# Optimization experiments

Measured on AMD Instinct MI355X. Metric: run time of the kernel, lower is better.

The kernel has to match this reference:

```python
import jax, jax.numpy as jnp
import numpy as np

B, C, H, W, A = 64, 1280, 7, 7, 40  # batch, in_features, spatial, num_attr


def h_swish(x):
    # x * relu6(x + 3) / 6
    return x * jnp.clip(x + 3.0, 0.0, 6.0) * (1.0 / 6.0)


def setup_inputs() -> dict:
    key = jax.random.key(0)
    kx, k1, k2, k3, k4 = jax.random.split(key, 5)
    s1 = 1.0 / np.sqrt(C)
    return {
        "x": jax.random.normal(kx, (B, C, H, W), dtype=jnp.float32),
        # batched per-attribute head params: Linear(C,C) then Linear(C,1)
        "W1": jax.random.uniform(k1, (A, C, C), jnp.float32, -s1, s1),
        "b1": jax.random.uniform(k2, (A, C), jnp.float32, -s1, s1),
        "W2": jax.random.uniform(k3, (A, C), jnp.float32, -s1, s1),
        "b2": jax.random.uniform(k4, (A,), jnp.float32, -s1, s1),
    }


def reference(x, W1, b1, W2, b2):
    # AdaptiveAvgPool2d((1,1)) + h_swish, then flatten -> [B, C]
    p = h_swish(jnp.mean(x, axis=(2, 3)))
    # all per-attribute heads as one batched GEMM: [B,C] x [A,C,C] -> [B,A,C]
    h = h_swish(jnp.einsum("bc,acd->bad", p, W1) + b1)
    # second layer: Linear(C,1) per attr -> [B, A]
    out = jnp.einsum("bac,ac->ba", h, W2) + b2
    # eval mode (self.training == False): sigmoid applied, dropout inactive
    return jax.nn.sigmoid(out)
```

## Files before the change

kernel.cpp:

```cpp
#include <hip/hip_runtime.h>
#include <hip/hip_bf16.h>

#define B_    64
#define C_    1280
#define HW_   49
#define A_    40
#define BN    128
#define BK    64
#define NKT   (C_/BK)
#define NTILE (C_/BN)

typedef short bf16x8 __attribute__((ext_vector_type(8)));
typedef float f32x4  __attribute__((ext_vector_type(4)));

__device__ __forceinline__ float hswish(float x) {
    float t = fminf(fmaxf(x + 3.0f, 0.0f), 6.0f);
    return x * t * (1.0f / 6.0f);
}

__device__ __forceinline__ short f2bf(float f) {
    __hip_bfloat16 h = __float2bfloat16(f);
    return __builtin_bit_cast(short, h);
}

__device__ __forceinline__ int swz(int r, int k) {
    return r * BK + ((((k >> 3) ^ r) & 7) << 3) + (k & 7);
}

#define POOL_ROWS 64
__global__ __launch_bounds__(256) void pool_kernel(const float* __restrict__ x,
                                                   __hip_bfloat16* __restrict__ p) {
    __shared__ float buf[POOL_ROWS * HW_];
    const int tid = threadIdx.x;
    const size_t base = (size_t)blockIdx.x * (POOL_ROWS * HW_);
    const float4* src = reinterpret_cast<const float4*>(x + base);
    #pragma unroll
    for (int i = 0; i < 3; ++i) {
        float4 v = src[tid + i * 256];
        *reinterpret_cast<float4*>(&buf[(tid + i * 256) * 4]) = v;
    }
    if (tid < 16) {
        float4 v = src[768 + tid];
        *reinterpret_cast<float4*>(&buf[(768 + tid) * 4]) = v;
    }
    __syncthreads();
    if (tid < POOL_ROWS) {
        float s = 0.f;
        #pragma unroll
        for (int j = 0; j < HW_; ++j) s += buf[tid * HW_ + j];
        s *= (1.0f / 49.0f);
        p[blockIdx.x * POOL_ROWS + tid] = __float2bfloat16(hswish(s));
    }
}

__global__ __launch_bounds__(256) void head_kernel(
    const short* __restrict__ p,
    const float* __restrict__ W1,
    const float* __restrict__ b1,
    const float* __restrict__ W2,
    float* __restrict__ part)
{
    __shared__ short w_lds[BN * BK];
    __shared__ short p_lds[B_ * BK];

    const int tid  = threadIdx.x;
    const int lane = tid & 63;
    const int wid  = tid >> 6;
    const int ntile = blockIdx.x;
    const int a     = blockIdx.y;
    const int n0    = ntile * BN;

    const int l15 = lane & 15;
    const int lg  = lane >> 4;

    const int sd = tid & 127;
    const int kh = (tid >> 7) * 32;
    const float* w1base = W1 + (size_t)a * C_ * C_ + n0 + sd;

    const int pr = tid & 63;
    const int ks = (tid >> 6) * 16;
    const short* pbase = p + (size_t)pr * C_ + ks;

    f32x4 acc[8];
    #pragma unroll
    for (int n = 0; n < 8; ++n) acc[n] = (f32x4){0.f, 0.f, 0.f, 0.f};

    float  wraw[32];
    bf16x8 praw[2];

#define LOADW(KT) do {                                              \
        const float* _wb = w1base + (size_t)((KT) * BK + kh) * C_;  \
        _Pragma("unroll")                                           \
        for (int _i = 0; _i < 32; ++_i)                             \
            wraw[_i] = _wb[(size_t)_i * C_];                        \
    } while (0)

#define LOADP(KT) do {                                              \
        const short* _pb = pbase + (KT) * BK;                       \
        praw[0] = *reinterpret_cast<const bf16x8*>(_pb);            \
        praw[1] = *reinterpret_cast<const bf16x8*>(_pb + 8);        \
    } while (0)

    LOADW(0); LOADP(0);

    for (int kt = 0; kt < NKT; ++kt) {
        __syncthreads();
        #pragma unroll
        for (int i = 0; i < 4; ++i) {
            bf16x8 v;
            #pragma unroll
            for (int j = 0; j < 8; ++j) v[j] = f2bf(wraw[i * 8 + j]);
            *reinterpret_cast<bf16x8*>(&w_lds[swz(sd, kh + i * 8)]) = v;
        }
        *reinterpret_cast<bf16x8*>(&p_lds[swz(pr, ks)])     = praw[0];
        *reinterpret_cast<bf16x8*>(&p_lds[swz(pr, ks + 8)]) = praw[1];
        __syncthreads();

        if (kt + 1 < NKT) { LOADW(kt + 1); LOADP(kt + 1); }

        #pragma unroll
        for (int h = 0; h < 2; ++h) {
            bf16x8 afrag = *reinterpret_cast<const bf16x8*>(
                &p_lds[swz(wid * 16 + l15, h * 32 + lg * 8)]);
            #pragma unroll
            for (int n = 0; n < 8; ++n) {
                bf16x8 bfrag = *reinterpret_cast<const bf16x8*>(
                    &w_lds[swz(n * 16 + l15, h * 32 + lg * 8)]);
                acc[n] = __builtin_amdgcn_mfma_f32_16x16x32_bf16(afrag, bfrag, acc[n], 0, 0, 0);
            }
        }
    }
#undef LOADW
#undef LOADP

    float partial[4] = {0.f, 0.f, 0.f, 0.f};
    #pragma unroll
    for (int n = 0; n < 8; ++n) {
        int col = n0 + n * 16 + l15;
        float b1v = b1[a * C_ + col];
        float w2v = W2[a * C_ + col];
        #pragma unroll
        for (int r = 0; r < 4; ++r)
            partial[r] += hswish(acc[n][r] + b1v) * w2v;
    }
    #pragma unroll
    for (int off = 8; off >= 1; off >>= 1)
        #pragma unroll
        for (int r = 0; r < 4; ++r)
            partial[r] += __shfl_xor(partial[r], off, 64);
    if (l15 == 0) {
        int brow = wid * 16 + lg * 4;
        #pragma unroll
        for (int r = 0; r < 4; ++r)
            part[ntile * (B_ * A_) + (brow + r) * A_ + a] = partial[r];
    }
}

__global__ __launch_bounds__(256) void fin_kernel(const float* __restrict__ part,
                                                  const float* __restrict__ b2,
                                                  float* __restrict__ out) {
    int idx = blockIdx.x * 256 + threadIdx.x;
    if (idx >= B_ * A_) return;
    int a = idx % A_;
    float s = b2[a];
    #pragma unroll
    for (int nb = 0; nb < NTILE; ++nb) s += part[nb * (B_ * A_) + idx];
    out[idx] = 1.0f / (1.0f + expf(-s));
}

extern "C" void kernel_launch(void* const* d_in, const int* in_sizes, int n_in,
                              void* d_out, int out_size, void* d_ws, size_t ws_size,
                              hipStream_t stream) {
    const float* x  = (const float*)d_in[0];
    const float* W1 = (const float*)d_in[1];
    const float* b1 = (const float*)d_in[2];
    const float* W2 = (const float*)d_in[3];
    const float* b2 = (const float*)d_in[4];
    float* out = (float*)d_out;

    __hip_bfloat16* p = (__hip_bfloat16*)d_ws;
    float* part = (float*)((char*)d_ws + (size_t)B_ * C_ * 2);

    pool_kernel<<<(B_ * C_) / POOL_ROWS, 256, 0, stream>>>(x, p);
    head_kernel<<<dim3(NTILE, A_), 256, 0, stream>>>((const short*)p, W1, b1, W2, part);
    fin_kernel<<<(B_ * A_ + 255) / 256, 256, 0, stream>>>(part, b2, out);
}
```

Measured before the change: 59.12 us.

## Halve head tile width and double-buffer register prefetch of W1 tiles

Narrows the N tile of the head GEMM from 128 to 64 columns, which doubles the grid to 800 blocks, and splits the register staging into two alternating buffers so global loads for two K-tiles ahead are in flight while the current tile is computed. Syncthreads is replaced by raw s_barrier plus an explicit lgkmcnt wait, and the per-wave partial sums are staged through a small LDS buffer before being written out. The goal is more memory-level parallelism on this bandwidth-bound fp32 weight stream. The cost is higher register pressure from the dropped launch bound, twice as many partial tiles for the final reduction, and barrier correctness that now depends on the manual waits.

```diff
diff --git a/kernel.cpp b/kernel.cpp
--- a/kernel.cpp
+++ b/kernel.cpp
@@ -5,7 +5,7 @@
 #define C_    1280
 #define HW_   49
 #define A_    40
-#define BN    128
+#define BN    64
 #define BK    64
 #define NKT   (C_/BK)
 #define NTILE (C_/BN)
@@ -53,7 +53,7 @@
     }
 }
 
-__global__ __launch_bounds__(256) void head_kernel(
+__global__ void head_kernel(
     const short* __restrict__ p,
     const float* __restrict__ W1,
     const float* __restrict__ b1,
@@ -62,6 +62,7 @@
 {
     __shared__ short w_lds[BN * BK];
     __shared__ short p_lds[B_ * BK];
+    __shared__ float red[4][B_];
 
     const int tid  = threadIdx.x;
     const int lane = tid & 63;
@@ -73,69 +74,86 @@
     const int l15 = lane & 15;
     const int lg  = lane >> 4;
 
-    const int sd = tid & 127;
-    const int kh = (tid >> 7) * 32;
+    const int sd = tid & 63;
+    const int kq = (tid >> 6) * 16;
     const float* w1base = W1 + (size_t)a * C_ * C_ + n0 + sd;
 
     const int pr = tid & 63;
     const int ks = (tid >> 6) * 16;
     const short* pbase = p + (size_t)pr * C_ + ks;
 
-    f32x4 acc[8];
-    #pragma unroll
-    for (int n = 0; n < 8; ++n) acc[n] = (f32x4){0.f, 0.f, 0.f, 0.f};
-
-    float  wraw[32];
-    bf16x8 praw[2];
-
-#define LOADW(KT) do {                                              \
-        const float* _wb = w1base + (size_t)((KT) * BK + kh) * C_;  \
+    f32x4 acc[4];
+    #pragma unroll
+    for (int n = 0; n < 4; ++n) acc[n] = (f32x4){0.f, 0.f, 0.f, 0.f};
+
+    float  wrawA[16], wrawB[16];
+    bf16x8 prawA[2], prawB[2];
+
+#define LOADW(KT, BUF) do {                                         \
+        const float* _wb = w1base + (size_t)((KT) * BK + kq) * C_;  \
         _Pragma("unroll")                                           \
-        for (int _i = 0; _i < 32; ++_i)                             \
-            wraw[_i] = _wb[(size_t)_i * C_];                        \
-    } while (0)
-
-#define LOADP(KT) do {                                              \
+        for (int _i = 0; _i < 16; ++_i)                             \
+            BUF[_i] = _wb[(size_t)_i * C_];                         \
+    } while (0)
+
+#define LOADP(KT, BUF) do {                                         \
         const short* _pb = pbase + (KT) * BK;                       \
-        praw[0] = *reinterpret_cast<const bf16x8*>(_pb);            \
-        praw[1] = *reinterpret_cast<const bf16x8*>(_pb + 8);        \
-    } while (0)
-
-    LOADW(0); LOADP(0);
-
-    for (int kt = 0; kt < NKT; ++kt) {
-        __syncthreads();
-        #pragma unroll
-        for (int i = 0; i < 4; ++i) {
-            bf16x8 v;
-            #pragma unroll
-            for (int j = 0; j < 8; ++j) v[j] = f2bf(wraw[i * 8 + j]);
-            *reinterpret_cast<bf16x8*>(&w_lds[swz(sd, kh + i * 8)]) = v;
-        }
-        *reinterpret_cast<bf16x8*>(&p_lds[swz(pr, ks)])     = praw[0];
-        *reinterpret_cast<bf16x8*>(&p_lds[swz(pr, ks + 8)]) = praw[1];
-        __syncthreads();
-
-        if (kt + 1 < NKT) { LOADW(kt + 1); LOADP(kt + 1); }
-
-        #pragma unroll
-        for (int h = 0; h < 2; ++h) {
-            bf16x8 afrag = *reinterpret_cast<const bf16x8*>(
-                &p_lds[swz(wid * 16 + l15, h * 32 + lg * 8)]);
-            #pragma unroll
-            for (int n = 0; n < 8; ++n) {
-                bf16x8 bfrag = *reinterpret_cast<const bf16x8*>(
-                    &w_lds[swz(n * 16 + l15, h * 32 + lg * 8)]);
-                acc[n] = __builtin_amdgcn_mfma_f32_16x16x32_bf16(afrag, bfrag, acc[n], 0, 0, 0);
-            }
-        }
+        BUF[0] = *reinterpret_cast<const bf16x8*>(_pb);             \
+        BUF[1] = *reinterpret_cast<const bf16x8*>(_pb + 8);         \
+    } while (0)
+
+#define STORE_TILE(WBUF, PBUF) do {                                 \
+        _Pragma("unroll")                                           \
+        for (int _i = 0; _i < 2; ++_i) {                            \
+            bf16x8 _v;                                              \
+            _Pragma("unroll")                                       \
+            for (int _j = 0; _j < 8; ++_j)                          \
+                _v[_j] = f2bf(WBUF[_i * 8 + _j]);                   \
+            *reinterpret_cast<bf16x8*>(&w_lds[swz(sd, kq + _i * 8)]) = _v; \
+        }                                                           \
+        *reinterpret_cast<bf16x8*>(&p_lds[swz(pr, ks)])     = PBUF[0]; \
+        *reinterpret_cast<bf16x8*>(&p_lds[swz(pr, ks + 8)]) = PBUF[1]; \
+    } while (0)
+
+#define COMPUTE() do {                                              \
+        _Pragma("unroll")                                           \
+        for (int _h = 0; _h < 2; ++_h) {                            \
+            bf16x8 _a = *reinterpret_cast<const bf16x8*>(           \
+                &p_lds[swz(wid * 16 + l15, _h * 32 + lg * 8)]);     \
+            _Pragma("unroll")                                       \
+            for (int _n = 0; _n < 4; ++_n) {                        \
+                bf16x8 _b = *reinterpret_cast<const bf16x8*>(       \
+                    &w_lds[swz(_n * 16 + l15, _h * 32 + lg * 8)]);  \
+                acc[_n] = __builtin_amdgcn_mfma_f32_16x16x32_bf16(_a, _b, acc[_n], 0, 0, 0); \
+            }                                                       \
+        }                                                           \
+    } while (0)
+
+    LOADW(0, wrawA); LOADP(0, prawA);
+    LOADW(1, wrawB); LOADP(1, prawB);
+
+    for (int t = 0; t < NKT; t += 2) {
+        __builtin_amdgcn_s_barrier();
+        STORE_TILE(wrawA, prawA);
+        asm volatile("s_waitcnt lgkmcnt(0)" ::: "memory");
+        __builtin_amdgcn_s_barrier();
+        if (t + 2 < NKT) { LOADW(t + 2, wrawA); LOADP(t + 2, prawA); }
+        COMPUTE();
+        __builtin_amdgcn_s_barrier();
+        STORE_TILE(wrawB, prawB);
+        asm volatile("s_waitcnt lgkmcnt(0)" ::: "memory");
+        __builtin_amdgcn_s_barrier();
+        if (t + 3 < NKT) { LOADW(t + 3, wrawB); LOADP(t + 3, prawB); }
+        COMPUTE();
     }
 #undef LOADW
 #undef LOADP
+#undef STORE_TILE
+#undef COMPUTE
 
     float partial[4] = {0.f, 0.f, 0.f, 0.f};
     #pragma unroll
-    for (int n = 0; n < 8; ++n) {
+    for (int n = 0; n < 4; ++n) {
         int col = n0 + n * 16 + l15;
         float b1v = b1[a * C_ + col];
         float w2v = W2[a * C_ + col];
@@ -152,7 +170,12 @@
         int brow = wid * 16 + lg * 4;
         #pragma unroll
         for (int r = 0; r < 4; ++r)
-            part[ntile * (B_ * A_) + (brow + r) * A_ + a] = partial[r];
+            red[wid][brow + r] = partial[r];
+    }
+    __syncthreads();
+    if (tid < B_) {
+        float s = red[tid >> 4][tid];
+        part[ntile * (B_ * A_) + tid * A_ + a] = s;
     }
 }
 
```

Result: slower. 73.69 us (+24.6%).
